# Optimization experiments

Hardware: AMD Instinct MI355X
Metric: run time of the kernel (lower is better)

Reference implementation:

```python
import jax, jax.numpy as jnp
import numpy as np
from jax import lax

B, FIN, FOUT, K, H, W = 4, 64, 64, 3, 128, 128


def setup_inputs() -> dict:
    key = jax.random.key(0)
    k1, k2, k3, k4, k5 = jax.random.split(key, 5)
    # fan-out per-channel conv weights: one KxK kernel per (out, in) pair
    fan = 1.0 / np.sqrt(K * K)  # torch Conv2d(1,1,K) init scale
    Wf = jax.random.uniform(k1, (FOUT, FIN, K, K), jnp.float32, -fan, fan)
    bf = jax.random.uniform(k2, (FOUT, FIN), jnp.float32, -fan, fan)
    # 1x1 combine: Conv2d(FIN, 1, 1) per output channel
    fc = 1.0 / np.sqrt(FIN)
    Wc = jax.random.uniform(k3, (FOUT, FIN), jnp.float32, -fc, fc)
    bc = jax.random.uniform(k4, (FOUT,), jnp.float32, -fc, fc)
    x = jax.random.normal(k5, (B, FIN, H, W), jnp.float32)
    return {"x": x, "Wf": Wf, "bf": bf, "Wc": Wc, "bc": bc}


def reference(x, Wf, bf, Wc, bc):
    fout, fin, k, _ = Wf.shape
    # Depthwise conv with channel multiplier fout: group i (input channel i)
    # produces output channels i*fout .. i*fout+fout-1, i.e. pair (i, o).
    kern = jnp.transpose(Wf, (2, 3, 1, 0)).reshape(k, k, 1, fin * fout)  # HWIO
    y = lax.conv_general_dilated(
        x, kern, window_strides=(1, 1), padding='VALID',
        dimension_numbers=('NCHW', 'HWIO', 'NCHW'),
        feature_group_count=fin)  # [B, fin*fout, H', W']
    y = y + bf.T.reshape(1, fin * fout, 1, 1)  # bias for pair (i, o)
    y = jax.nn.relu(y)
    b, _, h2, w2 = y.shape
    y = y.reshape(b, fin, fout, h2, w2)
    # 1x1 combine: out[b,o] = sum_i Wc[o,i] * y[b,i,o] + bc[o]
    out = jnp.einsum('biohw,oi->bohw', y, Wc) + bc[None, :, None, None]
    return out
```

## Files before the change

### kernel.cpp

```cpp
#include <hip/hip_runtime.h>

typedef _Float16 f16;
typedef f16 f16x4 __attribute__((ext_vector_type(4)));
typedef f16 f16x8 __attribute__((ext_vector_type(8)));
typedef float f32x4 __attribute__((ext_vector_type(4)));
typedef float f32x16 __attribute__((ext_vector_type(16)));
typedef unsigned int uint32;

#define FIN  64
#define FOUT 64
#define HI   128
#define WI   128
#define HO   126
#define WO   126
#define HIWI (HI*WI)
#define NPH  8
#define TR   8
#define TC   16
#define SR   10
#define SDW  12
#define CHSTR (SR*SDW)
#define NSLOT 8
#define XBUF (NSLOT*CHSTR)
#define NUNIT 400


__global__ __launch_bounds__(256) void prepass(
    const float* __restrict__ Wf, const float* __restrict__ bf,
    unsigned short* __restrict__ ws)
{
    int t = blockIdx.x * 256 + threadIdx.x;
    int i  = t >> 7;
    int ob = (t >> 6) & 1;
    int l  = t & 63;
    int g  = l >> 5, n = l & 31;
    int o  = ob * 32 + n;
    unsigned short h[8];
#pragma unroll
    for (int j = 0; j < 8; ++j) {
        int k = g * 4 + (j & 3) + 8 * (j >> 2);
        float v = 0.0f;
        if (k < 12) {
            int dy = k >> 2, dx = k & 3;
            if (dx < 3) v = Wf[((size_t)o * FIN + i) * 9 + dy * 3 + dx];
        } else if (k == 12) {
            v = bf[o * FIN + i];
        }
        f16 hv = (f16)v;
        h[j] = *(unsigned short*)&hv;
    }
    uint4 pk;
    pk.x = h[0] | ((uint32)h[1] << 16);
    pk.y = h[2] | ((uint32)h[3] << 16);
    pk.z = h[4] | ((uint32)h[5] << 16);
    pk.w = h[6] | ((uint32)h[7] << 16);
    *(uint4*)&ws[(size_t)t * 8] = pk;
}

__global__ __launch_bounds__(512, 4) void conv_mfma(
    const float* __restrict__ x,  const float* __restrict__ Wc,
    const float* __restrict__ bc, const unsigned short* __restrict__ ws,
    float* __restrict__ out)
{
    __shared__ __align__(16) union {
        struct { uint32 xsl[2][XBUF]; float wcl[32][68]; } a;
        float part[4][64][16];
        float ot[32][132];
    } sm;

    const int tid = threadIdx.x;
    const int l   = tid & 63, w = tid >> 6;
    const int wg  = w >> 2;
    const int wl  = w & 3;
    const int g   = l >> 5;
    const int m   = l & 31;
    const int prow = m >> 2;
    const int sx   = wl * 4 + (m & 3);
    const bool odd = (sx & 1);
    const int  qd  = sx >> 1;
    const int ibase = wg * 32;

    const int fid    = blockIdx.x;
    const int grp    = (fid >> 7) * 8 + (fid & 7);
    const int member = (fid >> 3) & 15;
    const int rx = grp & 15, b = grp >> 4;
    const int cy = member & 7, oh = member >> 3;
    const int row0 = rx * TR;
    const int col0 = cy * TC;
    const int o_lane = oh * 32 + m;

#pragma unroll
    for (int k = 0; k < 4; ++k) {
        int idx = tid + k * 512;
        sm.a.wcl[idx >> 6][idx & 63] =
            Wc[(size_t)(oh * 32 + (idx >> 6)) * FIN + (idx & 63)];
    }

    const float* xb = x + (size_t)b * FIN * HIWI;
    const bool stg = (tid < NUNIT);
    int slot = 0, goff = 0, widx = 0;
    if (stg) {
        slot = tid / 50;
        int rem = tid % 50;
        int r = rem / 5, u = rem % 5;
        int gy = min(row0 + r, HI - 1);
        int gx = min(col0 + 4 * u, WI - 4);
        goff = gy * WI + gx;
        widx = slot * CHSTR + r * SDW + 2 * u;
    }
    const int chbase = (slot >> 2) * 32 + (slot & 3);

    if (stg) {
        f32x4 v = *(const f32x4*)&xb[(size_t)chbase * HIWI + goff];
        f16x4 h; h[0] = (f16)v[0]; h[1] = (f16)v[1]; h[2] = (f16)v[2]; h[3] = (f16)v[3];
        *(uint2*)&sm.a.xsl[0][widx] = *(uint2*)&h;
    }

    const uint4* Btab = (const uint4*)ws;
    uint4 Bc[4], Bn[4];
#pragma unroll
    for (int c4 = 0; c4 < 4; ++c4)
        Bc[c4] = Btab[(size_t)((ibase + c4) * 2 + oh) * 64 + l];

    f32x16 acc = {}, zero = {};

    for (int ph = 0; ph < NPH; ++ph) {
        const int cur = ph & 1;
        const bool more = (ph + 1 < NPH);

        f32x4 sv = {};
        if (more) {
            if (stg) sv = *(const f32x4*)
                &xb[(size_t)(chbase + (ph + 1) * 4) * HIWI + goff];
#pragma unroll
            for (int c4 = 0; c4 < 4; ++c4)
                Bn[c4] = Btab[(size_t)((ibase + (ph + 1) * 4 + c4) * 2 + oh) * 64 + l];
        }

        __syncthreads();

        const f32x4 wcq = *(const f32x4*)&sm.a.wcl[m][ibase + ph * 4];
        const uint32* base = sm.a.xsl[cur];

#pragma unroll
        for (int c4 = 0; c4 < 4; ++c4) {
            const uint32* r1 = base + (wg * 4 + c4) * CHSTR + (prow + g) * SDW;
            const uint32* r2 = base + (wg * 4 + c4) * CHSTR + (prow + 2) * SDW;
            uint32 d0 = r1[qd], d1 = r1[qd + 1];
            uint32 e0 = r2[qd], e1 = r2[qd + 1];
            uint32 a0 = odd ? ((d0 >> 16) | (d1 << 16)) : d0;
            uint32 a1 = odd ? (d1 >> 16) : d1;
            uint32 b0 = odd ? ((e0 >> 16) | (e1 << 16)) : e0;
            uint32 b1 = odd ? (e1 >> 16) : e1;
            if (g) { b0 = 0x00003c00u; b1 = 0u; }
            uint4 auv = {a0, a1, b0, b1};
            f16x8 Af = *(f16x8*)&auv;
            f16x8 Bf = *(f16x8*)&Bc[c4];
            f32x16 S = __builtin_amdgcn_mfma_f32_32x32x16_f16(Af, Bf, zero, 0, 0, 0);
            const float wcv = wcq[c4];
#pragma unroll
            for (int r = 0; r < 16; ++r)
                acc[r] = fmaf(wcv, fmaxf(S[r], 0.0f), acc[r]);
        }

        if (more) {
            if (stg) {
                f16x4 h; h[0] = (f16)sv[0]; h[1] = (f16)sv[1];
                h[2] = (f16)sv[2]; h[3] = (f16)sv[3];
                *(uint2*)&sm.a.xsl[cur ^ 1][widx] = *(uint2*)&h;
            }
#pragma unroll
            for (int c4 = 0; c4 < 4; ++c4) Bc[c4] = Bn[c4];
        }
    }

    __syncthreads();
    if (wg == 1) {
#pragma unroll
        for (int r = 0; r < 16; ++r) sm.part[wl][l][r] = acc[r];
    }
    __syncthreads();
    if (wg == 0) {
#pragma unroll
        for (int r = 0; r < 16; ++r) acc[r] += sm.part[wl][l][r];
    }
    __syncthreads();

    if (wg == 0) {
        const float bcv = bc[o_lane];
#pragma unroll
        for (int r = 0; r < 16; ++r) {
            int p  = (r & 3) + 8 * (r >> 2) + 4 * g;
            int px = (p >> 2) * TC + wl * 4 + (p & 3);
            sm.ot[m][px] = acc[r] + bcv;
        }
    }
    __syncthreads();

    if (tid < 256) {
        const int oo  = tid >> 3;
        const int seg = tid & 7;
        const int o   = oh * 32 + oo;
        const int ho  = row0 + seg;
        if (ho < HO) {
            const float* src = &sm.ot[oo][seg * TC];
            size_t base = ((size_t)(b * FOUT + o) * HO + ho) * WO + col0;
            const int nst = (col0 + TC <= WO) ? TC : (WO - col0);
            for (int c = 0; c < nst; ++c) out[base + c] = src[c];
        }
    }
}

extern "C" void kernel_launch(void* const* d_in, const int* in_sizes, int n_in,
                              void* d_out, int out_size, void* d_ws, size_t ws_size,
                              hipStream_t stream) {
    const float* x  = (const float*)d_in[0];
    const float* Wf = (const float*)d_in[1];
    const float* bf = (const float*)d_in[2];
    const float* Wc = (const float*)d_in[3];
    const float* bc = (const float*)d_in[4];
    float* out = (float*)d_out;
    unsigned short* ws = (unsigned short*)d_ws;

    hipLaunchKernelGGL(prepass, dim3(32), dim3(256), 0, stream, Wf, bf, ws);

    hipLaunchKernelGGL(conv_mfma, dim3(1024), dim3(512), 0, stream,
                       x, Wc, bc, ws, out);
}
```

Measured before the change: 46.74 us.

## Use packed fp16 ReLU+dot2 combine, alignbit A-fragment build, prepacked Wc

The ReLU plus 1x1 combine epilogue now packs two channels' MFMA outputs into fp16 pairs and accumulates with a single fdot2 against fp16 Wc pairs. This halves the per-element VALU work that follows each MFMA. The pixel-to-lane mapping is changed so each lane's A fragment is built with alignbit from three dwords instead of odd/even shift selects, and a shared row of ones replaces the bias-row branch. Wc is converted to packed fp16 in the prepass, and staging is remapped to 50 lanes per wave with an unrolled output store. The cost is lower precision, since the intermediate activations are rounded to fp16 before the combine.

```diff
diff --git a/kernel.cpp b/kernel.cpp
--- a/kernel.cpp
+++ b/kernel.cpp
@@ -1,6 +1,7 @@
 #include <hip/hip_runtime.h>
 
 typedef _Float16 f16;
+typedef __fp16 h2 __attribute__((ext_vector_type(2)));
 typedef f16 f16x4 __attribute__((ext_vector_type(4)));
 typedef f16 f16x8 __attribute__((ext_vector_type(8)));
 typedef float f32x4 __attribute__((ext_vector_type(4)));
@@ -21,49 +22,58 @@
 #define SDW  12
 #define CHSTR (SR*SDW)
 #define NSLOT 8
-#define XBUF (NSLOT*CHSTR)
-#define NUNIT 400
+#define ONES_OFF (NSLOT*CHSTR)
+#define XBUF (ONES_OFF+SDW)
 
 
 __global__ __launch_bounds__(256) void prepass(
     const float* __restrict__ Wf, const float* __restrict__ bf,
-    unsigned short* __restrict__ ws)
+    const float* __restrict__ Wc, unsigned short* __restrict__ ws)
 {
     int t = blockIdx.x * 256 + threadIdx.x;
-    int i  = t >> 7;
-    int ob = (t >> 6) & 1;
-    int l  = t & 63;
-    int g  = l >> 5, n = l & 31;
-    int o  = ob * 32 + n;
-    unsigned short h[8];
-#pragma unroll
-    for (int j = 0; j < 8; ++j) {
-        int k = g * 4 + (j & 3) + 8 * (j >> 2);
-        float v = 0.0f;
-        if (k < 12) {
-            int dy = k >> 2, dx = k & 3;
-            if (dx < 3) v = Wf[((size_t)o * FIN + i) * 9 + dy * 3 + dx];
-        } else if (k == 12) {
-            v = bf[o * FIN + i];
-        }
-        f16 hv = (f16)v;
-        h[j] = *(unsigned short*)&hv;
-    }
-    uint4 pk;
-    pk.x = h[0] | ((uint32)h[1] << 16);
-    pk.y = h[2] | ((uint32)h[3] << 16);
-    pk.z = h[4] | ((uint32)h[5] << 16);
-    pk.w = h[6] | ((uint32)h[7] << 16);
-    *(uint4*)&ws[(size_t)t * 8] = pk;
+    if (t < 8192) {
+        int i  = t >> 7;
+        int ob = (t >> 6) & 1;
+        int l  = t & 63;
+        int g  = l >> 5, n = l & 31;
+        int o  = ob * 32 + n;
+        unsigned short h[8];
+#pragma unroll
+        for (int j = 0; j < 8; ++j) {
+            int k = g * 4 + (j & 3) + 8 * (j >> 2);
+            float v = 0.0f;
+            if (k < 12) {
+                int dy = k >> 2, dx = k & 3;
+                if (dx < 3) v = Wf[((size_t)o * FIN + i) * 9 + dy * 3 + dx];
+            } else if (k == 12) {
+                v = bf[o * FIN + i];
+            }
+            f16 hv = (f16)v;
+            h[j] = *(unsigned short*)&hv;
+        }
+        uint4 pk;
+        pk.x = h[0] | ((uint32)h[1] << 16);
+        pk.y = h[2] | ((uint32)h[3] << 16);
+        pk.z = h[4] | ((uint32)h[5] << 16);
+        pk.w = h[6] | ((uint32)h[7] << 16);
+        *(uint4*)&ws[(size_t)t * 8] = pk;
+    } else if (t < 8192 + 2048) {
+        int t2 = t - 8192;
+        int ip = t2 >> 6, o = t2 & 63;
+        f16 lo = (f16)Wc[(size_t)o * FIN + 2 * ip];
+        f16 hi = (f16)Wc[(size_t)o * FIN + 2 * ip + 1];
+        uint32 v = (uint32)*(unsigned short*)&lo |
+                   ((uint32)*(unsigned short*)&hi << 16);
+        ((uint32*)ws)[32768 + t2] = v;
+    }
 }
 
 __global__ __launch_bounds__(512, 4) void conv_mfma(
-    const float* __restrict__ x,  const float* __restrict__ Wc,
-    const float* __restrict__ bc, const unsigned short* __restrict__ ws,
-    float* __restrict__ out)
+    const float* __restrict__ x,  const float* __restrict__ bc,
+    const unsigned short* __restrict__ ws, float* __restrict__ out)
 {
     __shared__ __align__(16) union {
-        struct { uint32 xsl[2][XBUF]; float wcl[32][68]; } a;
+        struct { uint32 xsl[2][XBUF]; uint32 wcp[32][34]; } a;
         float part[4][64][16];
         float ot[32][132];
     } sm;
@@ -75,9 +85,8 @@
     const int g   = l >> 5;
     const int m   = l & 31;
     const int prow = m >> 2;
-    const int sx   = wl * 4 + (m & 3);
-    const bool odd = (sx & 1);
-    const int  qd  = sx >> 1;
+    const int qd   = (wl & 1) * 4 + (m & 3);
+    const int shl  = (wl >> 1) * 16;
     const int ibase = wg * 32;
 
     const int fid    = blockIdx.x;
@@ -89,26 +98,28 @@
     const int col0 = cy * TC;
     const int o_lane = oh * 32 + m;
 
-#pragma unroll
-    for (int k = 0; k < 4; ++k) {
-        int idx = tid + k * 512;
-        sm.a.wcl[idx >> 6][idx & 63] =
-            Wc[(size_t)(oh * 32 + (idx >> 6)) * FIN + (idx & 63)];
-    }
+    {
+        const uint32* wsrc = ((const uint32*)ws) + 32768;
+#pragma unroll
+        for (int k = 0; k < 2; ++k) {
+            int idx = tid + k * 512;
+            int oo = idx >> 5, ip = idx & 31;
+            sm.a.wcp[oo][ip] = wsrc[(size_t)ip * 64 + oh * 32 + oo];
+        }
+    }
+    if (tid < 2 * SDW) sm.a.xsl[tid / SDW][ONES_OFF + tid % SDW] = 0x3c003c00u;
 
     const float* xb = x + (size_t)b * FIN * HIWI;
-    const bool stg = (tid < NUNIT);
-    int slot = 0, goff = 0, widx = 0;
+    const bool stg = (l < 50);
+    int goff = 0, widx = 0;
     if (stg) {
-        slot = tid / 50;
-        int rem = tid % 50;
-        int r = rem / 5, u = rem % 5;
+        int r = l / 5, u = l % 5;
         int gy = min(row0 + r, HI - 1);
         int gx = min(col0 + 4 * u, WI - 4);
         goff = gy * WI + gx;
-        widx = slot * CHSTR + r * SDW + 2 * u;
-    }
-    const int chbase = (slot >> 2) * 32 + (slot & 3);
+        widx = w * CHSTR + r * SDW + 2 * u;
+    }
+    const int chbase = wg * 32 + wl;
 
     if (stg) {
         f32x4 v = *(const f32x4*)&xb[(size_t)chbase * HIWI + goff];
@@ -123,6 +134,11 @@
         Bc[c4] = Btab[(size_t)((ibase + c4) * 2 + oh) * 64 + l];
 
     f32x16 acc = {}, zero = {};
+    const h2 zh = {(__fp16)0.0f, (__fp16)0.0f};
+
+    const int r1off = (prow + g) * SDW + qd;
+    const int r2off = g ? (ONES_OFF + qd) : ((prow + 2) * SDW + qd);
+    const int r2str = g ? 0 : CHSTR;
 
     for (int ph = 0; ph < NPH; ++ph) {
         const int cur = ph & 1;
@@ -139,28 +155,49 @@
 
         __syncthreads();
 
-        const f32x4 wcq = *(const f32x4*)&sm.a.wcl[m][ibase + ph * 4];
+        const uint32 wcu0 = sm.a.wcp[m][wg * 16 + ph * 2];
+        const uint32 wcu1 = sm.a.wcp[m][wg * 16 + ph * 2 + 1];
         const uint32* base = sm.a.xsl[cur];
 
 #pragma unroll
-        for (int c4 = 0; c4 < 4; ++c4) {
-            const uint32* r1 = base + (wg * 4 + c4) * CHSTR + (prow + g) * SDW;
-            const uint32* r2 = base + (wg * 4 + c4) * CHSTR + (prow + 2) * SDW;
-            uint32 d0 = r1[qd], d1 = r1[qd + 1];
-            uint32 e0 = r2[qd], e1 = r2[qd + 1];
-            uint32 a0 = odd ? ((d0 >> 16) | (d1 << 16)) : d0;
-            uint32 a1 = odd ? (d1 >> 16) : d1;
-            uint32 b0 = odd ? ((e0 >> 16) | (e1 << 16)) : e0;
-            uint32 b1 = odd ? (e1 >> 16) : e1;
-            if (g) { b0 = 0x00003c00u; b1 = 0u; }
-            uint4 auv = {a0, a1, b0, b1};
-            f16x8 Af = *(f16x8*)&auv;
-            f16x8 Bf = *(f16x8*)&Bc[c4];
-            f32x16 S = __builtin_amdgcn_mfma_f32_32x32x16_f16(Af, Bf, zero, 0, 0, 0);
-            const float wcv = wcq[c4];
-#pragma unroll
-            for (int r = 0; r < 16; ++r)
-                acc[r] = fmaf(wcv, fmaxf(S[r], 0.0f), acc[r]);
+        for (int c2 = 0; c2 < 2; ++c2) {
+            const int ch0 = 2 * c2, ch1 = 2 * c2 + 1;
+            const uint32* r1a = base + (wg * 4 + ch0) * CHSTR + r1off;
+            const uint32* r2a = base + (wg * 4 + ch0) * r2str + r2off;
+            uint32 d0 = r1a[0], d1 = r1a[1], d2 = r1a[2];
+            uint32 e0 = r2a[0], e1 = r2a[1], e2 = r2a[2];
+            uint4 auv0 = {__builtin_amdgcn_alignbit(d1, d0, shl),
+                          __builtin_amdgcn_alignbit(d2, d1, shl),
+                          __builtin_amdgcn_alignbit(e1, e0, shl),
+                          __builtin_amdgcn_alignbit(e2, e1, shl)};
+            f16x8 Af0 = *(f16x8*)&auv0;
+            f32x16 S0 = __builtin_amdgcn_mfma_f32_32x32x16_f16(
+                            Af0, *(f16x8*)&Bc[ch0], zero, 0, 0, 0);
+
+            const uint32* r1b = base + (wg * 4 + ch1) * CHSTR + r1off;
+            const uint32* r2b = base + (wg * 4 + ch1) * r2str + r2off;
+            uint32 f0 = r1b[0], f1 = r1b[1], f2 = r1b[2];
+            uint32 k0 = r2b[0], k1 = r2b[1], k2 = r2b[2];
+            uint4 auv1 = {__builtin_amdgcn_alignbit(f1, f0, shl),
+                          __builtin_amdgcn_alignbit(f2, f1, shl),
+                          __builtin_amdgcn_alignbit(k1, k0, shl),
+                          __builtin_amdgcn_alignbit(k2, k1, shl)};
+            f16x8 Af1 = *(f16x8*)&auv1;
+            f32x16 S1 = __builtin_amdgcn_mfma_f32_32x32x16_f16(
+                            Af1, *(f16x8*)&Bc[ch1], zero, 0, 0, 0);
+
+            const uint32 wcu = c2 ? wcu1 : wcu0;
+            h2 wch;
+            {
+                uint32 t = wcu;
+                wch = *(h2*)&t;
+            }
+#pragma unroll
+            for (int r = 0; r < 16; ++r) {
+                h2 p = __builtin_amdgcn_cvt_pkrtz(S0[r], S1[r]);
+                p = __builtin_elementwise_max(p, zh);
+                acc[r] = __builtin_amdgcn_fdot2(p, wch, acc[r], false);
+            }
         }
 
         if (more) {
@@ -191,7 +228,7 @@
 #pragma unroll
         for (int r = 0; r < 16; ++r) {
             int p  = (r & 3) + 8 * (r >> 2) + 4 * g;
-            int px = (p >> 2) * TC + wl * 4 + (p & 3);
+            int px = (p >> 2) * TC + (wl & 1) * 8 + 2 * (p & 3) + (wl >> 1);
             sm.ot[m][px] = acc[r] + bcv;
         }
     }
@@ -205,8 +242,13 @@
         if (ho < HO) {
             const float* src = &sm.ot[oo][seg * TC];
             size_t base = ((size_t)(b * FOUT + o) * HO + ho) * WO + col0;
-            const int nst = (col0 + TC <= WO) ? TC : (WO - col0);
-            for (int c = 0; c < nst; ++c) out[base + c] = src[c];
+            if (col0 + TC <= WO) {
+#pragma unroll
+                for (int c = 0; c < TC; ++c) out[base + c] = src[c];
+            } else {
+#pragma unroll
+                for (int c = 0; c < 14; ++c) out[base + c] = src[c];
+            }
         }
     }
 }
@@ -222,8 +264,8 @@
     float* out = (float*)d_out;
     unsigned short* ws = (unsigned short*)d_ws;
 
-    hipLaunchKernelGGL(prepass, dim3(32), dim3(256), 0, stream, Wf, bf, ws);
+    hipLaunchKernelGGL(prepass, dim3(40), dim3(256), 0, stream, Wf, bf, Wc, ws);
 
     hipLaunchKernelGGL(conv_mfma, dim3(1024), dim3(512), 0, stream,
-                       x, Wc, bc, ws, out);
+                       x, bc, ws, out);
 }
```

New measurement: 44.54 us. 1.05x faster.
